# Kernel tuning notes

Measured on AMD Instinct MI355X. Metric: run time of the kernel, lower is better.

## Reference

```python
import jax, jax.numpy as jnp
import numpy as np

CODE_NUM = 64
IN_FEATURES = 3
CODE_CHANNEL = 64
SHAPE_NUM = 16


def setup_inputs() -> dict:
    key = jax.random.key(0)
    k1, k2, k3 = jax.random.split(key, 3)
    B, P = 8, 65536
    coords = jax.random.uniform(k1, (B, P, IN_FEATURES), dtype=jnp.float32)  # in [0,1) subset of [-1,1]
    idx = jax.random.randint(k2, (B,), 0, SHAPE_NUM, dtype=jnp.int32)
    # xavier_uniform for [C, shape_num*F*code_num]
    fan_in = SHAPE_NUM * IN_FEATURES * CODE_NUM
    bound = float(np.sqrt(6.0 / (CODE_CHANNEL + fan_in)))
    shape_code = jax.random.uniform(k3, (CODE_CHANNEL, fan_in), dtype=jnp.float32,
                                    minval=-bound, maxval=bound)
    return {"coords": coords, "idx": idx, "shape_code": shape_code}


def reference(coords, idx, shape_code):
    # coords: [B, P, F] in [-1, 1]; idx: [B] int; shape_code: [C, S*F*code_num]
    B, P, F = coords.shape
    C = shape_code.shape[0]
    # map to grid coordinates in [0, code_num-1]
    g = (coords + 1.0) * ((CODE_NUM - 1) / 2.0)                    # [B,P,F]
    corners = jnp.floor(g)[..., None] + jnp.array([0.0, 1.0], g.dtype)  # [B,P,F,2]
    coordsf = g[..., None] - corners                               # [B,P,F,2]
    weights = 1.0 - jnp.abs(coordsf)                               # [B,P,F,2]
    # flat codebook index: corner + feature offset + per-batch shape offset
    feat_off = (CODE_NUM * jnp.arange(F, dtype=jnp.int32))[:, None]        # [F,1]
    shape_off = (idx.astype(jnp.int32) * (CODE_NUM * F))[:, None, None, None]  # [B,1,1,1]
    index = corners.astype(jnp.int32) + feat_off + shape_off       # [B,P,F,2]
    # gather [B,P,F,2,C] then weighted reduce over (F,2)
    code_t = shape_code.T                                          # [S*F*code_num, C]
    gathered = code_t[index]                                       # [B,P,F,2,C]
    output = jnp.einsum('bpfkc,bpfk->bpc', gathered, weights)      # [B,P,C]
    return output
```

## Files before the change

kernel.cpp:

```cpp
#include <hip/hip_runtime.h>


#define CODE_NUM 64
#define NFEAT 3
#define NCHAN 64
#define NB 8
#define NP 65536
#define SLICE (CODE_NUM * NFEAT)
#define ROW_STRIDE 3072
#define NTHREADS 512
#define BLOCKS_PER_BATCH 64
#define PTS_PER_BLOCK (NP / BLOCKS_PER_BATCH)
#define PTS_PER_ITER (NTHREADS / 16)

__global__ __launch_bounds__(NTHREADS, 4)
void posenc_kernel(const float* __restrict__ coords,
                   const int* __restrict__ idx,
                   const float* __restrict__ shape_code,
                   float* __restrict__ out) {
    __shared__ float code_lds[SLICE * NCHAN];
    __shared__ float coord_lds[PTS_PER_BLOCK * NFEAT];

    const int bx    = blockIdx.x;
    const int b     = bx >> 6;
    const int chunk = (bx & (BLOCKS_PER_BATCH - 1)) * PTS_PER_BLOCK;
    const int tid   = threadIdx.x;
    const size_t bp0 = (size_t)b * NP;

    {
        const float4* src = reinterpret_cast<const float4*>(coords + (bp0 + chunk) * NFEAT);
        float4* dst = reinterpret_cast<float4*>(coord_lds);
        #pragma unroll
        for (int i = tid; i < PTS_PER_BLOCK * NFEAT / 4; i += NTHREADS)
            dst[i] = src[i];
    }

    const int base = idx[b] * SLICE;
    {
        const int c      = tid & 63;
        const int jchunk = tid >> 6;
        const float* src = shape_code + (size_t)c * ROW_STRIDE + base;
        #pragma unroll
        for (int jv = jchunk; jv < SLICE / 4; jv += NTHREADS / 64) {
            const float4 v = *reinterpret_cast<const float4*>(src + jv * 4);
            code_lds[(jv * 4 + 0) * NCHAN + c] = v.x;
            code_lds[(jv * 4 + 1) * NCHAN + c] = v.y;
            code_lds[(jv * 4 + 2) * NCHAN + c] = v.z;
            code_lds[(jv * 4 + 3) * NCHAN + c] = v.w;
        }
    }
    __syncthreads();

    const int gl   = tid & 15;
    const int pofs = tid >> 4;
    float* outg = out + (bp0 + chunk) * NCHAN + gl * 4;

    #pragma unroll 4
    for (int it = 0; it < PTS_PER_BLOCK / PTS_PER_ITER; ++it) {
        const int lp = it * PTS_PER_ITER + pofs;

        const float x0 = coord_lds[lp * 3 + 0];
        const float x1 = coord_lds[lp * 3 + 1];
        const float x2 = coord_lds[lp * 3 + 2];

        float4 acc = make_float4(0.f, 0.f, 0.f, 0.f);

        #pragma unroll
        for (int f = 0; f < NFEAT; ++f) {
            const float xf = (f == 0) ? x0 : (f == 1) ? x1 : x2;
            const float g  = (xf + 1.0f) * ((CODE_NUM - 1) * 0.5f);
            int c0 = (int)floorf(g);
            c0 = max(0, min(c0, CODE_NUM - 2));
            const float w1 = g - (float)c0;
            const float w0 = 1.0f - w1;

            const int r = (f * CODE_NUM + c0) * NCHAN + gl * 4;
            const float4 v0 = *reinterpret_cast<const float4*>(&code_lds[r]);
            const float4 v1 = *reinterpret_cast<const float4*>(&code_lds[r + NCHAN]);

            acc.x = fmaf(w0, v0.x, fmaf(w1, v1.x, acc.x));
            acc.y = fmaf(w0, v0.y, fmaf(w1, v1.y, acc.y));
            acc.z = fmaf(w0, v0.z, fmaf(w1, v1.z, acc.z));
            acc.w = fmaf(w0, v0.w, fmaf(w1, v1.w, acc.w));
        }

        *reinterpret_cast<float4*>(outg + (size_t)lp * NCHAN) = acc;
    }
}

extern "C" void kernel_launch(void* const* d_in, const int* in_sizes, int n_in,
                              void* d_out, int out_size, void* d_ws, size_t ws_size,
                              hipStream_t stream) {
    const float* coords     = (const float*)d_in[0];
    const int*   idx        = (const int*)d_in[1];
    const float* shape_code = (const float*)d_in[2];
    float*       out        = (float*)d_out;

    dim3 grid(NB * BLOCKS_PER_BATCH);
    dim3 block(NTHREADS);
    posenc_kernel<<<grid, block, 0, stream>>>(coords, idx, shape_code, out);
}
```

Before: 164.5 us.

## Software-pipeline LDS gathers and pad coords to float4 in LDS

Coordinates are staged in shared memory as padded float4 so each point needs a single LDS read instead of three scalar reads. The main loop is software-pipelined: the codebook rows for the next iteration are loaded while the current iteration's blend and store run, which is meant to hide LDS latency. The cost is higher register pressure from double-buffered float4s, a larger coord LDS footprint (16 KB vs 12 KB, which could reduce occupancy), and scalar uncoalesced global loads for coords.

```diff
diff --git a/kernel.cpp b/kernel.cpp
--- a/kernel.cpp
+++ b/kernel.cpp
@@ -12,14 +12,15 @@
 #define BLOCKS_PER_BATCH 64
 #define PTS_PER_BLOCK (NP / BLOCKS_PER_BATCH)
 #define PTS_PER_ITER (NTHREADS / 16)
+#define NIT (PTS_PER_BLOCK / PTS_PER_ITER)
 
 __global__ __launch_bounds__(NTHREADS, 4)
 void posenc_kernel(const float* __restrict__ coords,
                    const int* __restrict__ idx,
                    const float* __restrict__ shape_code,
                    float* __restrict__ out) {
-    __shared__ float code_lds[SLICE * NCHAN];
-    __shared__ float coord_lds[PTS_PER_BLOCK * NFEAT];
+    __shared__ float  code_lds[SLICE * NCHAN];
+    __shared__ float4 coord_lds[PTS_PER_BLOCK];
 
     const int bx    = blockIdx.x;
     const int b     = bx >> 6;
@@ -28,11 +29,10 @@
     const size_t bp0 = (size_t)b * NP;
 
     {
-        const float4* src = reinterpret_cast<const float4*>(coords + (bp0 + chunk) * NFEAT);
-        float4* dst = reinterpret_cast<float4*>(coord_lds);
+        const float* src = coords + (bp0 + chunk) * NFEAT;
         #pragma unroll
-        for (int i = tid; i < PTS_PER_BLOCK * NFEAT / 4; i += NTHREADS)
-            dst[i] = src[i];
+        for (int p = tid; p < PTS_PER_BLOCK; p += NTHREADS)
+            coord_lds[p] = make_float4(src[p * 3 + 0], src[p * 3 + 1], src[p * 3 + 2], 0.f);
     }
 
     const int base = idx[b] * SLICE;
@@ -55,37 +55,67 @@
     const int pofs = tid >> 4;
     float* outg = out + (bp0 + chunk) * NCHAN + gl * 4;
 
-    #pragma unroll 4
-    for (int it = 0; it < PTS_PER_BLOCK / PTS_PER_ITER; ++it) {
-        const int lp = it * PTS_PER_ITER + pofs;
+    const int inv0 = 0 * CODE_NUM * NCHAN + gl * 4;
+    const int inv1 = 1 * CODE_NUM * NCHAN + gl * 4;
+    const int inv2 = 2 * CODE_NUM * NCHAN + gl * 4;
 
-        const float x0 = coord_lds[lp * 3 + 0];
-        const float x1 = coord_lds[lp * 3 + 1];
-        const float x2 = coord_lds[lp * 3 + 2];
+#define LOAD_IT(IT, A0, A1, B0, B1, C0, C1, WA, WB, WC)                        \
+    {                                                                          \
+        const float4 xyz = coord_lds[(IT) * PTS_PER_ITER + pofs];              \
+        const float g0 = fmaf(xyz.x, 31.5f, 31.5f);                            \
+        const float g1 = fmaf(xyz.y, 31.5f, 31.5f);                            \
+        const float g2 = fmaf(xyz.z, 31.5f, 31.5f);                            \
+        int i0 = (int)floorf(g0); i0 = max(0, min(i0, CODE_NUM - 2));          \
+        int i1 = (int)floorf(g1); i1 = max(0, min(i1, CODE_NUM - 2));          \
+        int i2 = (int)floorf(g2); i2 = max(0, min(i2, CODE_NUM - 2));          \
+        WA = g0 - (float)i0;                                                   \
+        WB = g1 - (float)i1;                                                   \
+        WC = g2 - (float)i2;                                                   \
+        const float* r0 = &code_lds[inv0 + i0 * NCHAN];                        \
+        const float* r1 = &code_lds[inv1 + i1 * NCHAN];                        \
+        const float* r2 = &code_lds[inv2 + i2 * NCHAN];                        \
+        A0 = *reinterpret_cast<const float4*>(r0);                             \
+        A1 = *reinterpret_cast<const float4*>(r0 + NCHAN);                     \
+        B0 = *reinterpret_cast<const float4*>(r1);                             \
+        B1 = *reinterpret_cast<const float4*>(r1 + NCHAN);                     \
+        C0 = *reinterpret_cast<const float4*>(r2);                             \
+        C1 = *reinterpret_cast<const float4*>(r2 + NCHAN);                     \
+    }
 
-        float4 acc = make_float4(0.f, 0.f, 0.f, 0.f);
+#define COMPUTE_STORE(IT, A0, A1, B0, B1, C0, C1, WA, WB, WC)                  \
+    {                                                                          \
+        const float wa0 = 1.0f - WA, wb0 = 1.0f - WB, wc0 = 1.0f - WC;         \
+        float4 acc;                                                            \
+        acc.x = fmaf(wa0, A0.x, WA * A1.x);                                    \
+        acc.y = fmaf(wa0, A0.y, WA * A1.y);                                    \
+        acc.z = fmaf(wa0, A0.z, WA * A1.z);                                    \
+        acc.w = fmaf(wa0, A0.w, WA * A1.w);                                    \
+        acc.x = fmaf(wb0, B0.x, fmaf(WB, B1.x, acc.x));                        \
+        acc.y = fmaf(wb0, B0.y, fmaf(WB, B1.y, acc.y));                        \
+        acc.z = fmaf(wb0, B0.z, fmaf(WB, B1.z, acc.z));                        \
+        acc.w = fmaf(wb0, B0.w, fmaf(WB, B1.w, acc.w));                        \
+        acc.x = fmaf(wc0, C0.x, fmaf(WC, C1.x, acc.x));                        \
+        acc.y = fmaf(wc0, C0.y, fmaf(WC, C1.y, acc.y));                        \
+        acc.z = fmaf(wc0, C0.z, fmaf(WC, C1.z, acc.z));                        \
+        acc.w = fmaf(wc0, C0.w, fmaf(WC, C1.w, acc.w));                        \
+        *reinterpret_cast<float4*>(outg + (size_t)((IT) * PTS_PER_ITER + pofs) * NCHAN) = acc; \
+    }
 
-        #pragma unroll
-        for (int f = 0; f < NFEAT; ++f) {
-            const float xf = (f == 0) ? x0 : (f == 1) ? x1 : x2;
-            const float g  = (xf + 1.0f) * ((CODE_NUM - 1) * 0.5f);
-            int c0 = (int)floorf(g);
-            c0 = max(0, min(c0, CODE_NUM - 2));
-            const float w1 = g - (float)c0;
-            const float w0 = 1.0f - w1;
+    float4 A0, A1, B0, B1, C0, C1;
+    float  wA, wB, wC;
+    LOAD_IT(0, A0, A1, B0, B1, C0, C1, wA, wB, wC);
 
-            const int r = (f * CODE_NUM + c0) * NCHAN + gl * 4;
-            const float4 v0 = *reinterpret_cast<const float4*>(&code_lds[r]);
-            const float4 v1 = *reinterpret_cast<const float4*>(&code_lds[r + NCHAN]);
+    #pragma unroll 1
+    for (int it = 0; it < NIT - 1; ++it) {
+        const float4 a0 = A0, a1 = A1, b0 = B0, b1 = B1, c0 = C0, c1 = C1;
+        const float  wa = wA, wb = wB, wc = wC;
+        LOAD_IT(it + 1, A0, A1, B0, B1, C0, C1, wA, wB, wC);
+        COMPUTE_STORE(it, a0, a1, b0, b1, c0, c1, wa, wb, wc);
+    }
+    COMPUTE_STORE(NIT - 1, A0, A1, B0, B1, C0, C1, wA, wB, wC);
 
-            acc.x = fmaf(w0, v0.x, fmaf(w1, v1.x, acc.x));
-            acc.y = fmaf(w0, v0.y, fmaf(w1, v1.y, acc.y));
-            acc.z = fmaf(w0, v0.z, fmaf(w1, v1.z, acc.z));
-            acc.w = fmaf(w0, v0.w, fmaf(w1, v1.w, acc.w));
-        }
-
-        *reinterpret_cast<float4*>(outg + (size_t)lp * NCHAN) = acc;
-    }
+#undef LOAD_IT
+#undef COMPUTE_STORE
 }
 
 extern "C" void kernel_launch(void* const* d_in, const int* in_sizes, int n_in,
```

Result: no change. 162.6 us (-1.1%).

## Software-pipeline coord loads and LDS gathers, drop coord LDS staging

Applied to the files above, without the earlier changes.

Removes the LDS staging of coordinates and reads coords directly from global memory inside the loop. The main loop becomes a manually double-buffered pipeline that prefetches coords two iterations ahead and issues the LDS gathers one iteration ahead of the FMA and store. The aim is to hide global and LDS latency and cut the staging pass and LDS footprint. In exchange it uses more registers, and each thread issues three scattered scalar global loads per point, 16 lanes reading the same address.

```diff
diff --git a/kernel.cpp b/kernel.cpp
--- a/kernel.cpp
+++ b/kernel.cpp
@@ -12,6 +12,7 @@
 #define BLOCKS_PER_BATCH 64
 #define PTS_PER_BLOCK (NP / BLOCKS_PER_BATCH)
 #define PTS_PER_ITER (NTHREADS / 16)
+#define NIT (PTS_PER_BLOCK / PTS_PER_ITER)
 
 __global__ __launch_bounds__(NTHREADS, 4)
 void posenc_kernel(const float* __restrict__ coords,
@@ -19,21 +20,12 @@
                    const float* __restrict__ shape_code,
                    float* __restrict__ out) {
     __shared__ float code_lds[SLICE * NCHAN];
-    __shared__ float coord_lds[PTS_PER_BLOCK * NFEAT];
 
     const int bx    = blockIdx.x;
     const int b     = bx >> 6;
     const int chunk = (bx & (BLOCKS_PER_BATCH - 1)) * PTS_PER_BLOCK;
     const int tid   = threadIdx.x;
     const size_t bp0 = (size_t)b * NP;
-
-    {
-        const float4* src = reinterpret_cast<const float4*>(coords + (bp0 + chunk) * NFEAT);
-        float4* dst = reinterpret_cast<float4*>(coord_lds);
-        #pragma unroll
-        for (int i = tid; i < PTS_PER_BLOCK * NFEAT / 4; i += NTHREADS)
-            dst[i] = src[i];
-    }
 
     const int base = idx[b] * SLICE;
     {
@@ -53,39 +45,87 @@
 
     const int gl   = tid & 15;
     const int pofs = tid >> 4;
-    float* outg = out + (bp0 + chunk) * NCHAN + gl * 4;
+    const float* cp = coords + (bp0 + chunk) * NFEAT;
+    float*       og = out + (bp0 + chunk) * NCHAN + gl * 4;
 
-    #pragma unroll 4
-    for (int it = 0; it < PTS_PER_BLOCK / PTS_PER_ITER; ++it) {
-        const int lp = it * PTS_PER_ITER + pofs;
+    const int inv0 = 0 * CODE_NUM * NCHAN + gl * 4;
+    const int inv1 = 1 * CODE_NUM * NCHAN + gl * 4;
+    const int inv2 = 2 * CODE_NUM * NCHAN + gl * 4;
 
-        const float x0 = coord_lds[lp * 3 + 0];
-        const float x1 = coord_lds[lp * 3 + 1];
-        const float x2 = coord_lds[lp * 3 + 2];
+#define LOADC(IT, X0, X1, X2)                                                  \
+    {                                                                          \
+        const int _lp = (IT) * PTS_PER_ITER + pofs;                            \
+        X0 = cp[_lp * 3 + 0];                                                  \
+        X1 = cp[_lp * 3 + 1];                                                  \
+        X2 = cp[_lp * 3 + 2];                                                  \
+    }
 
-        float4 acc = make_float4(0.f, 0.f, 0.f, 0.f);
+#define ISSUE(X0, X1, X2, F0, F1, F2, F3, F4, F5, W0, W1, W2)                  \
+    {                                                                          \
+        const float g0 = fmaf(X0, 31.5f, 31.5f);                               \
+        const float g1 = fmaf(X1, 31.5f, 31.5f);                               \
+        const float g2 = fmaf(X2, 31.5f, 31.5f);                               \
+        int i0 = (int)floorf(g0); i0 = max(0, min(i0, CODE_NUM - 2));          \
+        int i1 = (int)floorf(g1); i1 = max(0, min(i1, CODE_NUM - 2));          \
+        int i2 = (int)floorf(g2); i2 = max(0, min(i2, CODE_NUM - 2));          \
+        W0 = g0 - (float)i0;                                                   \
+        W1 = g1 - (float)i1;                                                   \
+        W2 = g2 - (float)i2;                                                   \
+        const float* r0 = &code_lds[inv0 + i0 * NCHAN];                        \
+        const float* r1 = &code_lds[inv1 + i1 * NCHAN];                        \
+        const float* r2 = &code_lds[inv2 + i2 * NCHAN];                        \
+        F0 = *reinterpret_cast<const float4*>(r0);                             \
+        F1 = *reinterpret_cast<const float4*>(r0 + NCHAN);                     \
+        F2 = *reinterpret_cast<const float4*>(r1);                             \
+        F3 = *reinterpret_cast<const float4*>(r1 + NCHAN);                     \
+        F4 = *reinterpret_cast<const float4*>(r2);                             \
+        F5 = *reinterpret_cast<const float4*>(r2 + NCHAN);                     \
+    }
 
-        #pragma unroll
-        for (int f = 0; f < NFEAT; ++f) {
-            const float xf = (f == 0) ? x0 : (f == 1) ? x1 : x2;
-            const float g  = (xf + 1.0f) * ((CODE_NUM - 1) * 0.5f);
-            int c0 = (int)floorf(g);
-            c0 = max(0, min(c0, CODE_NUM - 2));
-            const float w1 = g - (float)c0;
-            const float w0 = 1.0f - w1;
+#define CONSUME(IT, F0, F1, F2, F3, F4, F5, W0, W1, W2)                        \
+    {                                                                          \
+        const float u0 = 1.0f - W0, u1 = 1.0f - W1, u2 = 1.0f - W2;            \
+        float4 acc;                                                            \
+        acc.x = fmaf(u0, F0.x, W0 * F1.x);                                     \
+        acc.y = fmaf(u0, F0.y, W0 * F1.y);                                     \
+        acc.z = fmaf(u0, F0.z, W0 * F1.z);                                     \
+        acc.w = fmaf(u0, F0.w, W0 * F1.w);                                     \
+        acc.x = fmaf(u1, F2.x, fmaf(W1, F3.x, acc.x));                         \
+        acc.y = fmaf(u1, F2.y, fmaf(W1, F3.y, acc.y));                         \
+        acc.z = fmaf(u1, F2.z, fmaf(W1, F3.z, acc.z));                         \
+        acc.w = fmaf(u1, F2.w, fmaf(W1, F3.w, acc.w));                         \
+        acc.x = fmaf(u2, F4.x, fmaf(W2, F5.x, acc.x));                         \
+        acc.y = fmaf(u2, F4.y, fmaf(W2, F5.y, acc.y));                         \
+        acc.z = fmaf(u2, F4.z, fmaf(W2, F5.z, acc.z));                         \
+        acc.w = fmaf(u2, F4.w, fmaf(W2, F5.w, acc.w));                         \
+        *reinterpret_cast<float4*>(og + (size_t)((IT) * PTS_PER_ITER + pofs) * NCHAN) = acc; \
+    }
 
-            const int r = (f * CODE_NUM + c0) * NCHAN + gl * 4;
-            const float4 v0 = *reinterpret_cast<const float4*>(&code_lds[r]);
-            const float4 v1 = *reinterpret_cast<const float4*>(&code_lds[r + NCHAN]);
+    float4 A0, A1, A2, A3, A4, A5, B0, B1, B2, B3, B4, B5;
+    float  wa0, wa1, wa2, wb0, wb1, wb2;
+    float  cA0, cA1, cA2, cB0, cB1, cB2;
 
-            acc.x = fmaf(w0, v0.x, fmaf(w1, v1.x, acc.x));
-            acc.y = fmaf(w0, v0.y, fmaf(w1, v1.y, acc.y));
-            acc.z = fmaf(w0, v0.z, fmaf(w1, v1.z, acc.z));
-            acc.w = fmaf(w0, v0.w, fmaf(w1, v1.w, acc.w));
-        }
+    LOADC(0, cA0, cA1, cA2);
+    LOADC(1, cB0, cB1, cB2);
+    ISSUE(cA0, cA1, cA2, A0, A1, A2, A3, A4, A5, wa0, wa1, wa2);
 
-        *reinterpret_cast<float4*>(outg + (size_t)lp * NCHAN) = acc;
+    #pragma unroll 1
+    for (int it = 0; it <= NIT - 4; it += 2) {
+        LOADC(it + 2, cA0, cA1, cA2);
+        ISSUE(cB0, cB1, cB2, B0, B1, B2, B3, B4, B5, wb0, wb1, wb2);
+        CONSUME(it, A0, A1, A2, A3, A4, A5, wa0, wa1, wa2);
+        LOADC(it + 3, cB0, cB1, cB2);
+        ISSUE(cA0, cA1, cA2, A0, A1, A2, A3, A4, A5, wa0, wa1, wa2);
+        CONSUME(it + 1, B0, B1, B2, B3, B4, B5, wb0, wb1, wb2);
     }
+
+    ISSUE(cB0, cB1, cB2, B0, B1, B2, B3, B4, B5, wb0, wb1, wb2);
+    CONSUME(NIT - 2, A0, A1, A2, A3, A4, A5, wa0, wa1, wa2);
+    CONSUME(NIT - 1, B0, B1, B2, B3, B4, B5, wb0, wb1, wb2);
+
+#undef LOADC
+#undef ISSUE
+#undef CONSUME
 }
 
 extern "C" void kernel_launch(void* const* d_in, const int* in_sizes, int n_in,
```

Result: faster. 151.2 us (-8.1%).
